# Kernel tuning notes

Measured on AMD Instinct MI355X. Metric: run time of the kernel, lower is better.

The kernel has to match this reference:

```python
import jax, jax.numpy as jnp
import numpy as np

B, S, H, N = 2, 2048, 1024, 16
HN = H // N  # head dim = 64
EPS = 1e-12


def setup_inputs() -> dict:
    key = jax.random.key(0)
    ks = jax.random.split(key, 8)
    scale = 0.02
    return {
        "hidden_states": jax.random.normal(ks[0], (B, S, H), dtype=jnp.float32),
        "attention_mask": jnp.zeros((B, 1, 1, S), dtype=jnp.float32),
        "W_qkv": jax.random.normal(ks[1], (3 * H, H), dtype=jnp.float32) * scale,
        "b_qkv": jnp.zeros((3 * H,), dtype=jnp.float32),
        "W_out": jax.random.normal(ks[2], (H, H), dtype=jnp.float32) * scale,
        "b_out": jnp.zeros((H,), dtype=jnp.float32),
        "ln_gamma": jnp.ones((H,), dtype=jnp.float32),
        "ln_beta": jnp.zeros((H,), dtype=jnp.float32),
    }


def reference(hidden_states, attention_mask, W_qkv, b_qkv, W_out, b_out, ln_gamma, ln_beta):
    # QKV projection: torch Linear => x @ W.T + b
    qkv = jnp.einsum("bsh,oh->bso", hidden_states, W_qkv) + b_qkv  # [B,S,3H]
    q, k, v = jnp.split(qkv, 3, axis=-1)

    def heads(t):  # [B,S,H] -> [B,N,S,HN]
        return t.reshape(B, S, N, HN).transpose(0, 2, 1, 3)

    q, k, v = heads(q), heads(k), heads(v)
    nf = jnp.sqrt(jnp.sqrt(jnp.float32(HN)))
    scores = jnp.einsum("bnsd,bntd->bnst", q / nf, k / nf) + attention_mask  # [B,N,S,S]
    probs = jax.nn.softmax(scores, axis=-1)
    ctx = jnp.einsum("bnst,bntd->bnsd", probs, v)  # [B,N,S,HN]
    ctx = ctx.transpose(0, 2, 1, 3).reshape(B, S, H)

    # output dense + residual + LayerNorm
    out = jnp.einsum("bsh,oh->bso", ctx, W_out) + b_out
    x = out + hidden_states
    mean = jnp.mean(x, axis=-1, keepdims=True)
    var = jnp.mean(jnp.square(x - mean), axis=-1, keepdims=True)
    return (x - mean) * jax.lax.rsqrt(var + EPS) * ln_gamma + ln_beta
```

## Files before the change

kernel.cpp:

```cpp
#include <hip/hip_runtime.h>
#include <hip/hip_bf16.h>
#include <math.h>

#define Bq  2
#define Sq  2048
#define Hq  1024
#define Nq  16
#define HNq 64
#define Mq  (Bq*Sq)
#define H3q (3*Hq)

#define LOG2E 1.44269504088896340736f

typedef __attribute__((ext_vector_type(8))) short           short8;
typedef __attribute__((ext_vector_type(4))) short           short4s;
typedef __attribute__((ext_vector_type(8))) unsigned short  ushortx8;
typedef __attribute__((ext_vector_type(4))) unsigned short  ushortx4;
typedef __attribute__((ext_vector_type(4))) float           floatx4;

__device__ __forceinline__ unsigned short f2bf(float f) {
    union { float f; unsigned int u; } x; x.f = f;
    unsigned int r = (x.u + 0x7fffu + ((x.u >> 16) & 1u)) >> 16;
    return (unsigned short)r;
}

__device__ __forceinline__ unsigned int pkbf(float a, float b) {
    float2 t; t.x = a; t.y = b;
    __hip_bfloat162 h = __float22bfloat162_rn(t);
    union { __hip_bfloat162 h; unsigned int u; } c; c.h = h;
    return c.u;
}

__device__ __forceinline__ float bf2f(unsigned short v) {
    union { unsigned int u; float f; } x; x.u = (unsigned int)v << 16;
    return x.f;
}

__device__ __forceinline__ float fexp2(float x) {
    float r;
    asm("v_exp_f32 %0, %1" : "=v"(r) : "v"(x));
    return r;
}

__device__ __forceinline__ void gload16(const unsigned short* g, unsigned short* l) {
    __builtin_amdgcn_global_load_lds(
        (__attribute__((address_space(1))) void*)(unsigned long long)(g),
        (__attribute__((address_space(3))) void*)(unsigned int)(unsigned long long)(l),
        16, 0, 0);
}

__device__ __forceinline__ int swz(int r) { return (r ^ (r >> 2)) & 3; }

#define N_HID ((size_t)Mq * Hq)
#define N_HW  (N_HID + (size_t)H3q * Hq)
#define N_ALL (N_HW + (size_t)Hq * Hq)
#define CVT_BLKS ((int)(N_ALL / 2048))

__global__ __launch_bounds__(256) void cvt_all(
    const float* __restrict__ hidden, const float* __restrict__ wqkv,
    const float* __restrict__ wout, const float* __restrict__ mask,
    unsigned short* __restrict__ dst, unsigned short* __restrict__ em2)
{
    const int bid = blockIdx.x;
    if (bid >= CVT_BLKS) {
        const int t0   = ((bid - CVT_BLKS) * 256 + threadIdx.x) * 8;
        const int b    = t0 >> 11;
        const int t2   = t0 & 2047;
        const int kt   = t2 >> 6;
        const int t3   = t2 & 63;
        const int ks   = t3 >> 5;
        const int quad = (t3 >> 3) & 3;
        const int kb   = kt * 64 + ks * 32 + quad * 4;
        const float* mp = mask + (size_t)b * Sq + kb;
        float4 m0 = *(const float4*)(mp);
        float4 m1 = *(const float4*)(mp + 16);
        union { unsigned int u[4]; ushortx8 s; } o;
        o.u[0] = pkbf(fexp2(m0.x * LOG2E), fexp2(m0.y * LOG2E));
        o.u[1] = pkbf(fexp2(m0.z * LOG2E), fexp2(m0.w * LOG2E));
        o.u[2] = pkbf(fexp2(m1.x * LOG2E), fexp2(m1.y * LOG2E));
        o.u[3] = pkbf(fexp2(m1.z * LOG2E), fexp2(m1.w * LOG2E));
        *(ushortx8*)(em2 + t0) = o.s;
        return;
    }
    size_t i = ((size_t)bid * 256 + threadIdx.x) * 8;
    const float* src;
    if (i < N_HID)      src = hidden + i;
    else if (i < N_HW)  src = wqkv + (i - N_HID);
    else                src = wout + (i - N_HW);
    float4 a = *(const float4*)(src);
    float4 b = *(const float4*)(src + 4);
    union { unsigned int u[4]; ushortx8 s; } o;
    o.u[0] = pkbf(a.x, a.y); o.u[1] = pkbf(a.z, a.w);
    o.u[2] = pkbf(b.x, b.y); o.u[3] = pkbf(b.z, b.w);
    *(ushortx8*)(dst + i) = o.s;
}

#define TM 128
#define TN 128
#define TK 32
#define G1M 256

__global__ __launch_bounds__(512) void gemm_mfma_qkv(
    const unsigned short* __restrict__ A, const unsigned short* __restrict__ Bw,
    const float* __restrict__ bias, const float* __restrict__ mask,
    unsigned short* __restrict__ Qb, unsigned short* __restrict__ KV5, int K)
{
    __shared__ unsigned short As[3][G1M][TK];
    __shared__ unsigned short Bs[3][TN][TK];

    const int tid = threadIdx.x;
    const int w = tid >> 6, lane = tid & 63;
    const int l15 = lane & 15, quad = lane >> 4;
    const int wr = (w & 3) * 64;
    const int wc = (w >> 2) * 64;
    const int row0 = blockIdx.y * G1M;
    const int col0 = blockIdx.x * TN;

    const int srow16 = lane >> 2;
    const int sgd    = lane & 3;
    const int sgsrc  = (sgd ^ swz(srow16)) * 8;

    floatx4 acc[4][4];
    #pragma unroll
    for (int i = 0; i < 4; i++)
        #pragma unroll
        for (int j = 0; j < 4; j++) acc[i][j] = (floatx4){0.f,0.f,0.f,0.f};

    const int aswz = swz(l15) * 8;
    const int NK = K / TK;

    #pragma unroll
    for (int t = 0; t < 2; t++) {
        #pragma unroll
        for (int c = 0; c < 2; c++) {
            int seg = w * 2 + c;
            int r = seg * 16 + srow16;
            gload16(A + (size_t)(row0 + r) * K + t * TK + sgsrc, &As[t][seg * 16][0]);
        }
        int rB = w * 16 + srow16;
        gload16(Bw + (size_t)(col0 + rB) * K + t * TK + sgsrc, &Bs[t][w * 16][0]);
    }

    #pragma unroll 1
    for (int k = 0; k < NK; ++k) {
        if (k + 1 < NK) asm volatile("s_waitcnt vmcnt(3)" ::: "memory");
        else            asm volatile("s_waitcnt vmcnt(0)" ::: "memory");
        __builtin_amdgcn_s_barrier();
        __builtin_amdgcn_sched_barrier(0);

        const int cur = k % 3;
        if (k + 2 < NK) {
            const int nb  = (k + 2) % 3;
            const int k0n = (k + 2) * TK;
            #pragma unroll
            for (int c = 0; c < 2; c++) {
                int seg = w * 2 + c;
                int r = seg * 16 + srow16;
                gload16(A + (size_t)(row0 + r) * K + k0n + sgsrc, &As[nb][seg * 16][0]);
            }
            int rB = w * 16 + srow16;
            gload16(Bw + (size_t)(col0 + rB) * K + k0n + sgsrc, &Bs[nb][w * 16][0]);
        }
        __builtin_amdgcn_sched_barrier(0);

        short8 af[4], bf[4];
        #pragma unroll
        for (int i = 0; i < 4; i++)
            af[i] = *(const short8*)&As[cur][wr + i * 16 + l15][(quad * 8) ^ aswz];
        #pragma unroll
        for (int j = 0; j < 4; j++)
            bf[j] = *(const short8*)&Bs[cur][wc + j * 16 + l15][(quad * 8) ^ aswz];
        __builtin_amdgcn_s_setprio(1);
        #pragma unroll
        for (int i = 0; i < 4; i++)
            #pragma unroll
            for (int j = 0; j < 4; j++)
                acc[i][j] = __builtin_amdgcn_mfma_f32_16x16x32_bf16(af[i], bf[j], acc[i][j], 0, 0, 0);
        __builtin_amdgcn_s_setprio(0);
    }

    const int cls = col0 >> 10;

    if (cls == 2) {
        #pragma unroll
        for (int i = 0; i < 4; i++) {
            const int rb = row0 + wr + i * 16 + quad * 4;
            const int b  = rb >> 11;
            const int s  = rb & (Sq - 1);
            const int kt32 = s >> 6;
            const int sw   = s & 63;
            const int kg   = sw >> 2;
            const int ks   = kg >> 3;
            const int q2   = kg & 3;
            const int hi   = (kg >> 2) & 1;
            float expm[4];
            #pragma unroll
            for (int rr = 0; rr < 4; rr++)
                expm[rr] = fexp2(mask[(size_t)b * Sq + s + rr] * LOG2E);
            #pragma unroll
            for (int j = 0; j < 4; j++) {
                const int c  = col0 + wc + j * 16 + l15;
                const int c2 = c - 2 * Hq;
                const int n  = c2 >> 6, d = c2 & 63;
                const int dt = d >> 4, dl = d & 15;
                const float bia = bias[c];
                ushortx4 o;
                #pragma unroll
                for (int rr = 0; rr < 4; rr++)
                    o[rr] = f2bf((acc[i][j][rr] + bia) * expm[rr]);
                const size_t off = (((size_t)(b * Nq + n) * 32 + kt32) << 13) + 4096
                                 + (size_t)((ks * 16 + dt * 4 + q2) * 128 + dl * 8 + hi * 4);
                *(ushortx4*)&KV5[off] = o;
            }
        }
    } else if (cls == 1) {
        #pragma unroll
        for (int i = 0; i < 4; i++) {
            const int rb = row0 + wr + i * 16 + quad * 4;
            #pragma unroll
            for (int j = 0; j < 4; j++) {
                const int c  = col0 + wc + j * 16 + l15;
                const int c2 = c - Hq;
                const int n  = c2 >> 6, d = c2 & 63;
                const float bia = bias[c];
                #pragma unroll
                for (int rr = 0; rr < 4; rr++) {
                    const int srow = rb + rr;
                    const int b    = srow >> 11;
                    const int s    = srow & (Sq - 1);
                    const int kt32 = s >> 6;
                    const int r    = s & 63;
                    const size_t off = (((size_t)(b * Nq + n) * 32 + kt32) << 13)
                                     + (size_t)(r * 64 + (((d >> 3) ^ (r & 7)) * 8 + (d & 7)));
                    KV5[off] = f2bf(acc[i][j][rr] + bia);
                }
            }
        }
    } else {
        const float qs = 0.125f * LOG2E;
        #pragma unroll
        for (int i = 0; i < 4; i++) {
            const int rb = row0 + wr + i * 16 + quad * 4;
            #pragma unroll
            for (int j = 0; j < 4; j++) {
                const int c = col0 + wc + j * 16 + l15;
                const float bia = bias[c];
                #pragma unroll
                for (int rr = 0; rr < 4; rr++)
                    Qb[(size_t)(rb + rr) * Hq + c] =
                        f2bf((acc[i][j][rr] + bia) * qs);
            }
        }
    }
}

#define T2M 64
#define T2N 128

__global__ __launch_bounds__(256) void gemm_mfma_out(
    const unsigned short* __restrict__ A, const unsigned short* __restrict__ Bw,
    const float* __restrict__ bias, const float* __restrict__ res,
    unsigned short* __restrict__ X, int M, int Nd, int K)
{
    __shared__ unsigned short As[3][T2M][TK];
    __shared__ unsigned short Bs[3][T2N][TK];

    const int tid = threadIdx.x;
    const int w = tid >> 6, lane = tid & 63;
    const int l15 = lane & 15, quad = lane >> 4;
    const int wr = (w & 1) * 32;
    const int wc = (w >> 1) * 64;
    const int row0 = blockIdx.y * T2M;
    const int col0 = blockIdx.x * T2N;

    const int srow16 = lane >> 2;
    const int sgd    = lane & 3;
    const int sgsrc  = (sgd ^ swz(srow16)) * 8;

    floatx4 acc[2][4];
    #pragma unroll
    for (int i = 0; i < 2; i++)
        #pragma unroll
        for (int j = 0; j < 4; j++) acc[i][j] = (floatx4){0.f,0.f,0.f,0.f};

    const int aswz = swz(l15) * 8;
    const int NK = K / TK;

    #pragma unroll
    for (int t = 0; t < 2; t++) {
        int rA = w * 16 + srow16;
        gload16(A + (size_t)(row0 + rA) * K + t * TK + sgsrc, &As[t][w * 16][0]);
        #pragma unroll
        for (int c = 0; c < 2; c++) {
            int seg = w * 2 + c;
            int rB = seg * 16 + srow16;
            gload16(Bw + (size_t)(col0 + rB) * K + t * TK + sgsrc, &Bs[t][seg * 16][0]);
        }
    }

    #pragma unroll 1
    for (int k = 0; k < NK; ++k) {
        if (k + 1 < NK) asm volatile("s_waitcnt vmcnt(3)" ::: "memory");
        else            asm volatile("s_waitcnt vmcnt(0)" ::: "memory");
        __builtin_amdgcn_s_barrier();
        __builtin_amdgcn_sched_barrier(0);

        const int cur = k % 3;
        if (k + 2 < NK) {
            const int nb  = (k + 2) % 3;
            const int k0n = (k + 2) * TK;
            int rA = w * 16 + srow16;
            gload16(A + (size_t)(row0 + rA) * K + k0n + sgsrc, &As[nb][w * 16][0]);
            #pragma unroll
            for (int c = 0; c < 2; c++) {
                int seg = w * 2 + c;
                int rB = seg * 16 + srow16;
                gload16(Bw + (size_t)(col0 + rB) * K + k0n + sgsrc, &Bs[nb][seg * 16][0]);
            }
        }
        __builtin_amdgcn_sched_barrier(0);

        short8 af[2], bf[4];
        #pragma unroll
        for (int i = 0; i < 2; i++)
            af[i] = *(const short8*)&As[cur][wr + i * 16 + l15][(quad * 8) ^ aswz];
        #pragma unroll
        for (int j = 0; j < 4; j++)
            bf[j] = *(const short8*)&Bs[cur][wc + j * 16 + l15][(quad * 8) ^ aswz];
        __builtin_amdgcn_s_setprio(1);
        #pragma unroll
        for (int i = 0; i < 2; i++)
            #pragma unroll
            for (int j = 0; j < 4; j++)
                acc[i][j] = __builtin_amdgcn_mfma_f32_16x16x32_bf16(af[i], bf[j], acc[i][j], 0, 0, 0);
        __builtin_amdgcn_s_setprio(0);
    }

    #pragma unroll
    for (int i = 0; i < 2; i++) {
        const int rb = row0 + wr + i * 16 + quad * 4;
        #pragma unroll
        for (int j = 0; j < 4; j++) {
            const int c = col0 + wc + j * 16 + l15;
            const float bia = bias[c];
            #pragma unroll
            for (int rr = 0; rr < 4; rr++) {
                X[(size_t)(rb + rr) * Nd + c] =
                    f2bf(acc[i][j][rr] + bia + res[(size_t)(rb + rr) * Nd + c]);
            }
        }
    }
}

#define KTILES 32

__device__ __forceinline__ floatx4 mfma16(short8 a, short8 b, floatx4 c) {
    return __builtin_amdgcn_mfma_f32_16x16x32_bf16(a, b, c, 0, 0, 0);
}

__device__ __forceinline__ void do_lpv(
    const short8 (&pf0)[2], const short8 (&pf1)[2], const short8 (&mf)[2],
    const unsigned short* Vt,
    floatx4 (&oacc0)[4], floatx4 (&oacc1)[4],
    floatx4 &lacc0, floatx4 &lacc1)
{
    __builtin_amdgcn_s_setprio(1);
    lacc0 = mfma16(mf[0], pf0[0], lacc0);
    lacc0 = mfma16(mf[1], pf0[1], lacc0);
    lacc1 = mfma16(mf[0], pf1[0], lacc1);
    lacc1 = mfma16(mf[1], pf1[1], lacc1);
    #pragma unroll
    for (int dt = 0; dt < 4; dt++) {
        short8 vlo = *(const short8*)(Vt + dt * 512);
        short8 vhi = *(const short8*)(Vt + 2048 + dt * 512);
        oacc0[dt] = mfma16(vlo, pf0[0], oacc0[dt]);
        oacc1[dt] = mfma16(vlo, pf1[0], oacc1[dt]);
        oacc0[dt] = mfma16(vhi, pf0[1], oacc0[dt]);
        oacc1[dt] = mfma16(vhi, pf1[1], oacc1[dt]);
    }
    __builtin_amdgcn_s_setprio(0);
}

template<bool HAVER, bool PREF>
__device__ __forceinline__ void attn_body(
    int kt,
    unsigned short (&KsL)[2][64][64],
    unsigned short (&VsL)[3][4096],
    const unsigned short* KVb, const unsigned short* e2b,
    int w, int l15, int quad, int lane,
    const short8 (&qf0)[2], const short8 (&qf1)[2],
    const short8 (&pfR0)[2], const short8 (&pfR1)[2], const short8 (&mfR)[2],
    short8 (&pfW0)[2], short8 (&pfW1)[2], short8 (&mfW)[2],
    floatx4 (&oacc0)[4], floatx4 (&oacc1)[4],
    floatx4 &lacc0, floatx4 &lacc1)
{
    asm volatile("s_waitcnt vmcnt(0)" ::: "memory");
    __builtin_amdgcn_s_barrier();
    __builtin_amdgcn_sched_barrier(0);

    if (PREF) {
        const unsigned short* tb = KVb + (size_t)(kt + 1) * 8192 + w * 1024 + lane * 8;
        gload16(tb,        &KsL[(kt + 1) & 1][w * 16][0]);
        gload16(tb + 512,  &KsL[(kt + 1) & 1][w * 16 + 8][0]);
        unsigned short* vd = &VsL[(kt + 1) % 3][w * 1024];
        gload16(tb + 4096,       vd);
        gload16(tb + 4096 + 512, vd + 512);
    }
    __builtin_amdgcn_sched_barrier(0);

    const unsigned short* ep = e2b + kt * 64;
    mfW[0] = *(const short8*)(ep + quad * 8);
    mfW[1] = *(const short8*)(ep + 32 + quad * 8);

    floatx4 s0[4], s1[4];
    #pragma unroll
    for (int ct = 0; ct < 4; ct++) {
        s0[ct] = (floatx4){0.f,0.f,0.f,0.f};
        s1[ct] = (floatx4){0.f,0.f,0.f,0.f};
    }
    __builtin_amdgcn_s_setprio(1);
    #pragma unroll
    for (int ks = 0; ks < 2; ks++) {
        #pragma unroll
        for (int ct = 0; ct < 4; ct++) {
            short8 af = *(const short8*)&KsL[kt & 1][ct * 16 + l15][((4 * ks + quad) ^ (l15 & 7)) * 8];
            s0[ct] = mfma16(af, qf0[ks], s0[ct]);
            s1[ct] = mfma16(af, qf1[ks], s1[ct]);
        }
    }
    __builtin_amdgcn_s_setprio(0);

    #pragma unroll
    for (int ks = 0; ks < 2; ks++) {
        union { unsigned int u[4]; short8 s; } pk;
        #pragma unroll
        for (int h = 0; h < 2; h++) {
            const int ct = ks * 2 + h;
            pk.u[h * 2]     = pkbf(fexp2(s0[ct][0]), fexp2(s0[ct][1]));
            pk.u[h * 2 + 1] = pkbf(fexp2(s0[ct][2]), fexp2(s0[ct][3]));
        }
        pfW0[ks] = pk.s;
    }
    #pragma unroll
    for (int ks = 0; ks < 2; ks++) {
        union { unsigned int u[4]; short8 s; } pk;
        #pragma unroll
        for (int h = 0; h < 2; h++) {
            const int ct = ks * 2 + h;
            pk.u[h * 2]     = pkbf(fexp2(s1[ct][0]), fexp2(s1[ct][1]));
            pk.u[h * 2 + 1] = pkbf(fexp2(s1[ct][2]), fexp2(s1[ct][3]));
        }
        pfW1[ks] = pk.s;
    }

    if (HAVER)
        do_lpv(pfR0, pfR1, mfR, &VsL[(kt - 1) % 3][0] + lane * 8,
               oacc0, oacc1, lacc0, lacc1);
}

__global__ __launch_bounds__(256) void attn_mfma(
    const unsigned short* __restrict__ Qb, const unsigned short* __restrict__ KV5,
    const unsigned short* __restrict__ em2, unsigned short* __restrict__ ctx)
{
    __shared__ unsigned short Ks[2][64][64];
    __shared__ unsigned short Vs[3][4096];

    const int tid  = threadIdx.x;
    const int w    = tid >> 6;
    const int lane = tid & 63;
    const int l15  = lane & 15;
    const int quad = lane >> 4;

    const int i_    = blockIdx.x;
    const int gl8   = i_ & 7;
    const int rest  = i_ >> 3;
    const int qtile = rest & 15;
    const int g     = (rest >> 4) * 8 + gl8;
    const int n     = g & 15;
    const int b     = g >> 4;

    short8 qf0[2], qf1[2];
    {
        const int qrow0 = qtile * 128 + w * 16 + l15;
        const unsigned short* qp = Qb + (size_t)(b * Sq + qrow0) * Hq + n * HNq + quad * 8;
        qf0[0] = *(const short8*)(qp);
        qf0[1] = *(const short8*)(qp + 32);
        qp += (size_t)64 * Hq;
        qf1[0] = *(const short8*)(qp);
        qf1[1] = *(const short8*)(qp + 32);
    }

    floatx4 oacc0[4], oacc1[4];
    #pragma unroll
    for (int dt = 0; dt < 4; dt++) {
        oacc0[dt] = (floatx4){0.f,0.f,0.f,0.f};
        oacc1[dt] = (floatx4){0.f,0.f,0.f,0.f};
    }
    floatx4 lacc0 = (floatx4){0.f,0.f,0.f,0.f};
    floatx4 lacc1 = (floatx4){0.f,0.f,0.f,0.f};

    const unsigned short* KVb = KV5 + (size_t)(b * Nq + n) * 32 * 8192;
    const unsigned short* e2b = em2 + (size_t)b * 32 * 64;

    {
        const unsigned short* tb = KVb + w * 1024 + lane * 8;
        gload16(tb,        &Ks[0][w * 16][0]);
        gload16(tb + 512,  &Ks[0][w * 16 + 8][0]);
        gload16(tb + 4096,       &Vs[0][w * 1024]);
        gload16(tb + 4096 + 512, &Vs[0][w * 1024] + 512);
    }

    short8 pfA0[2], pfA1[2], mfA[2];
    short8 pfB0[2], pfB1[2], mfB[2];

    attn_body<false, true>(0, Ks, Vs, KVb, e2b, w, l15, quad, lane,
        qf0, qf1, pfB0, pfB1, mfB, pfA0, pfA1, mfA, oacc0, oacc1, lacc0, lacc1);

    #pragma unroll 1
    for (int kt = 1; kt < KTILES - 1; kt += 2) {
        attn_body<true, true>(kt, Ks, Vs, KVb, e2b, w, l15, quad, lane,
            qf0, qf1, pfA0, pfA1, mfA, pfB0, pfB1, mfB, oacc0, oacc1, lacc0, lacc1);
        attn_body<true, true>(kt + 1, Ks, Vs, KVb, e2b, w, l15, quad, lane,
            qf0, qf1, pfB0, pfB1, mfB, pfA0, pfA1, mfA, oacc0, oacc1, lacc0, lacc1);
    }
    attn_body<true, false>(KTILES - 1, Ks, Vs, KVb, e2b, w, l15, quad, lane,
        qf0, qf1, pfA0, pfA1, mfA, pfB0, pfB1, mfB, oacc0, oacc1, lacc0, lacc1);
    do_lpv(pfB0, pfB1, mfB, &Vs[(KTILES - 1) % 3][0] + lane * 8,
           oacc0, oacc1, lacc0, lacc1);

    #pragma unroll
    for (int sub = 0; sub < 2; sub++) {
        const float inv = 1.0f / (sub ? lacc1[0] : lacc0[0]);
        const int qrow = qtile * 128 + sub * 64 + w * 16 + l15;
        #pragma unroll
        for (int dt = 0; dt < 4; dt++) {
            const floatx4 oa = sub ? oacc1[dt] : oacc0[dt];
            union { unsigned int u[2]; ushortx4 s; } o;
            o.u[0] = pkbf(oa[0] * inv, oa[1] * inv);
            o.u[1] = pkbf(oa[2] * inv, oa[3] * inv);
            const int col = n * HNq + dt * 16 + quad * 4;
            *(ushortx4*)&ctx[(size_t)(b * Sq + qrow) * Hq + col] = o.s;
        }
    }
}

__global__ __launch_bounds__(256) void ln_kernel(
    const unsigned short* __restrict__ X, const float* __restrict__ gamma,
    const float* __restrict__ beta, float* __restrict__ out)
{
    const int row = blockIdx.x;
    const int c0  = threadIdx.x * 4;
    ushortx4 xv = *(const ushortx4*)(X + (size_t)row * Hq + c0);
    float vals[4];
    float lsum = 0.0f;
    #pragma unroll
    for (int i = 0; i < 4; i++) { vals[i] = bf2f(xv[i]); lsum += vals[i]; }

    __shared__ float red[8];
    const int wid = threadIdx.x >> 6, lane = threadIdx.x & 63;

    float s = lsum;
    #pragma unroll
    for (int off = 32; off >= 1; off >>= 1) s += __shfl_xor(s, off, 64);
    if (lane == 0) red[wid] = s;
    __syncthreads();
    const float mean = (red[0] + red[1] + red[2] + red[3]) * (1.0f / Hq);

    float v = 0.0f;
    #pragma unroll
    for (int i = 0; i < 4; i++) { float d = vals[i] - mean; v += d * d; }
    #pragma unroll
    for (int off = 32; off >= 1; off >>= 1) v += __shfl_xor(v, off, 64);
    if (lane == 0) red[4 + wid] = v;
    __syncthreads();
    const float var  = (red[4] + red[5] + red[6] + red[7]) * (1.0f / Hq);
    const float rstd = rsqrtf(var + 1e-12f);

    float4 gm = *(const float4*)(gamma + c0);
    float4 bt = *(const float4*)(beta + c0);
    float4 o;
    o.x = (vals[0] - mean) * rstd * gm.x + bt.x;
    o.y = (vals[1] - mean) * rstd * gm.y + bt.y;
    o.z = (vals[2] - mean) * rstd * gm.z + bt.z;
    o.w = (vals[3] - mean) * rstd * gm.w + bt.w;
    *(float4*)(out + (size_t)row * Hq + c0) = o;
}

extern "C" void kernel_launch(void* const* d_in, const int* in_sizes, int n_in,
                              void* d_out, int out_size, void* d_ws, size_t ws_size,
                              hipStream_t stream)
{
    const float* hidden = (const float*)d_in[0];
    const float* mask   = (const float*)d_in[1];
    const float* W_qkv  = (const float*)d_in[2];
    const float* b_qkv  = (const float*)d_in[3];
    const float* W_out  = (const float*)d_in[4];
    const float* b_out  = (const float*)d_in[5];
    const float* gamma  = (const float*)d_in[6];
    const float* beta   = (const float*)d_in[7];
    float* out = (float*)d_out;

    const size_t nHid  = (size_t)Mq * Hq;
    const size_t nWq   = (size_t)H3q * Hq;
    const size_t nWo   = (size_t)Hq * Hq;

    unsigned short* hidden_bf = (unsigned short*)d_ws;
    unsigned short* Wqkv_bf   = hidden_bf + nHid;
    unsigned short* Wout_bf   = Wqkv_bf + nWq;
    unsigned short* qb        = Wout_bf + nWo;
    unsigned short* kv5       = qb + nHid;
    unsigned short* ctx_bf    = kv5 + 2 * nHid;
    unsigned short* x_bf      = ctx_bf + nHid;
    unsigned short* em2       = x_bf + nHid;

    dim3 blk(256);

    cvt_all<<<dim3(CVT_BLKS + 2), blk, 0, stream>>>(
        hidden, W_qkv, W_out, mask, hidden_bf, em2);

    gemm_mfma_qkv<<<dim3(H3q / TN, Mq / G1M), dim3(512), 0, stream>>>(
        hidden_bf, Wqkv_bf, b_qkv, mask, qb, kv5, Hq);

    attn_mfma<<<dim3(512), blk, 0, stream>>>(
        qb, kv5, em2, ctx_bf);

    gemm_mfma_out<<<dim3(Hq / T2N, Mq / T2M), blk, 0, stream>>>(
        ctx_bf, Wout_bf, b_out, hidden, x_bf, Mq, Hq, Hq);

    ln_kernel<<<dim3(Mq), blk, 0, stream>>>(x_bf, gamma, beta, out);
}
```

Measured before the change: 193.7 us.

## Deepen attention K/V prefetch to two tiles ahead with partial vmcnt waits

The attention kernel now prefetches K/V tiles two iterations ahead instead of one. K gets triple buffering and V gets quad buffering in LDS, and the full vmcnt(0) drain is replaced with vmcnt(4) so the next tile's loads can stay in flight across the barrier. The goal is to hide global-load latency behind more compute. The cost is more LDS per block (about 56KB instead of 40KB), which may reduce occupancy, plus a more complex prologue and epilogue.

```diff
diff --git a/kernel.cpp b/kernel.cpp
--- a/kernel.cpp
+++ b/kernel.cpp
@@ -381,11 +381,11 @@
     __builtin_amdgcn_s_setprio(0);
 }
 
-template<bool HAVER, bool PREF>
+template<bool HAVER, bool PREF2, int VW>
 __device__ __forceinline__ void attn_body(
     int kt,
-    unsigned short (&KsL)[2][64][64],
-    unsigned short (&VsL)[3][4096],
+    unsigned short (&KsL)[3][64][64],
+    unsigned short (&VsL)[4][4096],
     const unsigned short* KVb, const unsigned short* e2b,
     int w, int l15, int quad, int lane,
     const short8 (&qf0)[2], const short8 (&qf1)[2],
@@ -394,23 +394,24 @@
     floatx4 (&oacc0)[4], floatx4 (&oacc1)[4],
     floatx4 &lacc0, floatx4 &lacc1)
 {
-    asm volatile("s_waitcnt vmcnt(0)" ::: "memory");
+    asm volatile("s_waitcnt vmcnt(%0)" :: "i"(VW) : "memory");
     __builtin_amdgcn_s_barrier();
-    __builtin_amdgcn_sched_barrier(0);
-
-    if (PREF) {
-        const unsigned short* tb = KVb + (size_t)(kt + 1) * 8192 + w * 1024 + lane * 8;
-        gload16(tb,        &KsL[(kt + 1) & 1][w * 16][0]);
-        gload16(tb + 512,  &KsL[(kt + 1) & 1][w * 16 + 8][0]);
-        unsigned short* vd = &VsL[(kt + 1) % 3][w * 1024];
-        gload16(tb + 4096,       vd);
-        gload16(tb + 4096 + 512, vd + 512);
-    }
     __builtin_amdgcn_sched_barrier(0);
 
     const unsigned short* ep = e2b + kt * 64;
     mfW[0] = *(const short8*)(ep + quad * 8);
     mfW[1] = *(const short8*)(ep + 32 + quad * 8);
+    __builtin_amdgcn_sched_barrier(0);
+
+    if (PREF2) {
+        const unsigned short* tb = KVb + (size_t)(kt + 2) * 8192 + w * 1024 + lane * 8;
+        gload16(tb,       &KsL[(kt + 2) % 3][w * 16][0]);
+        gload16(tb + 512, &KsL[(kt + 2) % 3][w * 16 + 8][0]);
+        unsigned short* vd = &VsL[(kt + 2) & 3][w * 1024];
+        gload16(tb + 4096,       vd);
+        gload16(tb + 4096 + 512, vd + 512);
+    }
+    __builtin_amdgcn_sched_barrier(0);
 
     floatx4 s0[4], s1[4];
     #pragma unroll
@@ -423,7 +424,7 @@
     for (int ks = 0; ks < 2; ks++) {
         #pragma unroll
         for (int ct = 0; ct < 4; ct++) {
-            short8 af = *(const short8*)&KsL[kt & 1][ct * 16 + l15][((4 * ks + quad) ^ (l15 & 7)) * 8];
+            short8 af = *(const short8*)&KsL[kt % 3][ct * 16 + l15][((4 * ks + quad) ^ (l15 & 7)) * 8];
             s0[ct] = mfma16(af, qf0[ks], s0[ct]);
             s1[ct] = mfma16(af, qf1[ks], s1[ct]);
         }
@@ -454,7 +455,7 @@
     }
 
     if (HAVER)
-        do_lpv(pfR0, pfR1, mfR, &VsL[(kt - 1) % 3][0] + lane * 8,
+        do_lpv(pfR0, pfR1, mfR, &VsL[(kt + 3) & 3][0] + lane * 8,
                oacc0, oacc1, lacc0, lacc1);
 }
 
@@ -462,8 +463,8 @@
     const unsigned short* __restrict__ Qb, const unsigned short* __restrict__ KV5,
     const unsigned short* __restrict__ em2, unsigned short* __restrict__ ctx)
 {
-    __shared__ unsigned short Ks[2][64][64];
-    __shared__ unsigned short Vs[3][4096];
+    __shared__ unsigned short Ks[3][64][64];
+    __shared__ unsigned short Vs[4][4096];
 
     const int tid  = threadIdx.x;
     const int w    = tid >> 6;
@@ -502,30 +503,35 @@
     const unsigned short* KVb = KV5 + (size_t)(b * Nq + n) * 32 * 8192;
     const unsigned short* e2b = em2 + (size_t)b * 32 * 64;
 
-    {
-        const unsigned short* tb = KVb + w * 1024 + lane * 8;
-        gload16(tb,        &Ks[0][w * 16][0]);
-        gload16(tb + 512,  &Ks[0][w * 16 + 8][0]);
-        gload16(tb + 4096,       &Vs[0][w * 1024]);
-        gload16(tb + 4096 + 512, &Vs[0][w * 1024] + 512);
+    #pragma unroll
+    for (int t = 0; t < 2; t++) {
+        const unsigned short* tb = KVb + (size_t)t * 8192 + w * 1024 + lane * 8;
+        gload16(tb,        &Ks[t][w * 16][0]);
+        gload16(tb + 512,  &Ks[t][w * 16 + 8][0]);
+        gload16(tb + 4096,       &Vs[t][w * 1024]);
+        gload16(tb + 4096 + 512, &Vs[t][w * 1024] + 512);
     }
 
     short8 pfA0[2], pfA1[2], mfA[2];
     short8 pfB0[2], pfB1[2], mfB[2];
 
-    attn_body<false, true>(0, Ks, Vs, KVb, e2b, w, l15, quad, lane,
+    attn_body<false, true, 4>(0, Ks, Vs, KVb, e2b, w, l15, quad, lane,
         qf0, qf1, pfB0, pfB1, mfB, pfA0, pfA1, mfA, oacc0, oacc1, lacc0, lacc1);
 
     #pragma unroll 1
-    for (int kt = 1; kt < KTILES - 1; kt += 2) {
-        attn_body<true, true>(kt, Ks, Vs, KVb, e2b, w, l15, quad, lane,
+    for (int kt = 1; kt < KTILES - 3; kt += 2) {
+        attn_body<true, true, 4>(kt, Ks, Vs, KVb, e2b, w, l15, quad, lane,
             qf0, qf1, pfA0, pfA1, mfA, pfB0, pfB1, mfB, oacc0, oacc1, lacc0, lacc1);
-        attn_body<true, true>(kt + 1, Ks, Vs, KVb, e2b, w, l15, quad, lane,
+        attn_body<true, true, 4>(kt + 1, Ks, Vs, KVb, e2b, w, l15, quad, lane,
             qf0, qf1, pfB0, pfB1, mfB, pfA0, pfA1, mfA, oacc0, oacc1, lacc0, lacc1);
     }
-    attn_body<true, false>(KTILES - 1, Ks, Vs, KVb, e2b, w, l15, quad, lane,
+    attn_body<true, true, 4>(KTILES - 3, Ks, Vs, KVb, e2b, w, l15, quad, lane,
         qf0, qf1, pfA0, pfA1, mfA, pfB0, pfB1, mfB, oacc0, oacc1, lacc0, lacc1);
-    do_lpv(pfB0, pfB1, mfB, &Vs[(KTILES - 1) % 3][0] + lane * 8,
+    attn_body<true, false, 4>(KTILES - 2, Ks, Vs, KVb, e2b, w, l15, quad, lane,
+        qf0, qf1, pfB0, pfB1, mfB, pfA0, pfA1, mfA, oacc0, oacc1, lacc0, lacc1);
+    attn_body<true, false, 0>(KTILES - 1, Ks, Vs, KVb, e2b, w, l15, quad, lane,
+        qf0, qf1, pfA0, pfA1, mfA, pfB0, pfB1, mfB, oacc0, oacc1, lacc0, lacc1);
+    do_lpv(pfB0, pfB1, mfB, &Vs[(KTILES - 1) & 3][0] + lane * 8,
            oacc0, oacc1, lacc0, lacc1);
 
     #pragma unroll
```

After: 195.4 us. About the same (+0.9%).
